# Optimization experiments

Measured on AMD Instinct MI355X. Metric: run time of the kernel, lower is better.

The kernel has to match this reference:

```python
import jax, jax.numpy as jnp
import numpy as np

H = W = 32
CROP = int(H * 0.8)  # 25, matches int(H*crop_ratio) in torch
MEAN = jnp.array([0.5071, 0.4867, 0.4408], jnp.float32).reshape(1, 3, 1, 1)
STD = jnp.array([0.2675, 0.2565, 0.2761], jnp.float32).reshape(1, 3, 1, 1)


def _bilinear(img, iy, ix):
    # img [C,H,W]; iy/ix [H,W] float pixel coords (reflected+clamped already)
    y0 = jnp.floor(iy); x0 = jnp.floor(ix)
    wy = iy - y0; wx = ix - x0
    y0i = jnp.clip(y0.astype(jnp.int32), 0, H - 1); y1i = jnp.clip(y0i + 1, 0, H - 1)
    x0i = jnp.clip(x0.astype(jnp.int32), 0, W - 1); x1i = jnp.clip(x0i + 1, 0, W - 1)
    v00 = img[:, y0i, x0i]; v01 = img[:, y0i, x1i]
    v10 = img[:, y1i, x0i]; v11 = img[:, y1i, x1i]
    return v00 * (1 - wy) * (1 - wx) + v01 * (1 - wy) * wx + v10 * wy * (1 - wx) + v11 * wy * wx


def _reflect(c, size):
    # PyTorch grid_sample reflection padding, align_corners=False (reflect about -0.5 / size-0.5)
    lo = -0.5
    span = float(size)
    t = jnp.abs(c - lo)
    extra = jnp.mod(t, span)
    flips = jnp.floor(t / span)
    out = jnp.where(jnp.mod(flips, 2.0) == 0.0, lo + extra, lo + span - extra)
    return jnp.clip(out, 0.0, size - 1.0)


def _crop_resize_one(img, top, left):
    # bilinear resize of img[:, top:top+CROP, left:left+CROP] -> HxW, align_corners=False
    d = (jnp.arange(W, dtype=jnp.float32) + 0.5) * (CROP / W) - 0.5
    d = jnp.maximum(d, 0.0)
    i0 = jnp.floor(d).astype(jnp.int32)
    lam = d - i0
    i1 = jnp.minimum(i0 + 1, CROP - 1)
    r0 = top + i0; r1 = top + i1; c0 = left + i0; c1 = left + i1
    v00 = img[:, r0[:, None], c0[None, :]]
    v01 = img[:, r0[:, None], c1[None, :]]
    v10 = img[:, r1[:, None], c0[None, :]]
    v11 = img[:, r1[:, None], c1[None, :]]
    ly = lam[:, None]; lx = lam[None, :]
    return v00 * (1 - ly) * (1 - lx) + v01 * (1 - ly) * lx + v10 * ly * (1 - lx) + v11 * ly * lx


def _grid_sample_one(img, theta):
    # affine_grid + grid_sample (bilinear, reflection, align_corners=False)
    xs = (2.0 * (jnp.arange(W, dtype=jnp.float32) + 0.5) / W) - 1.0
    ys = (2.0 * (jnp.arange(H, dtype=jnp.float32) + 0.5) / H) - 1.0
    yn, xn = jnp.meshgrid(ys, xs, indexing='ij')
    gx = theta[0, 0] * xn + theta[0, 1] * yn + theta[0, 2]
    gy = theta[1, 0] * xn + theta[1, 1] * yn + theta[1, 2]
    ix = _reflect(((gx + 1.0) * W - 1.0) * 0.5, W)
    iy = _reflect(((gy + 1.0) * H - 1.0) * 0.5, H)
    return _bilinear(img, iy, ix)


def _augment(x, shared_affine, apply_crop):
    B = x.shape[0]
    ks = jax.random.split(jax.random.key(42), 10)
    x = x * STD + MEAN  # de-normalize
    if apply_crop:
        max_off = H - CROP
        top = jax.random.randint(ks[0], (B,), 0, max_off + 1)
        left = jax.random.randint(ks[1], (B,), 0, max_off + 1)
        x = jax.vmap(_crop_resize_one)(x, top, left)
    flip_mask = jax.random.uniform(ks[2], (B,)) < 0.5
    x = jnp.where(flip_mask[:, None, None, None], x[..., ::-1], x)
    # shared affine is provided -> always applied (torch shared_affine branch)
    x = jax.vmap(_grid_sample_one)(x, shared_affine)
    brightness = 1.0 + (jax.random.uniform(ks[3], (B, 1, 1, 1)) - 0.5) * 0.8
    x = x * brightness
    gray = x.mean(axis=1, keepdims=True)
    contrast = 1.0 + (jax.random.uniform(ks[4], (B, 1, 1, 1)) - 0.5) * 0.8
    x = gray + (x - gray) * contrast
    gray = x.mean(axis=1, keepdims=True)
    saturation = 1.0 + (jax.random.uniform(ks[5], (B, 1, 1, 1)) - 0.5) * 0.8
    x = gray + (x - gray) * saturation
    hue_mask = jax.random.uniform(ks[6], (B,)) < 0.5
    x = jnp.where(hue_mask[:, None, None, None], x[:, ::-1], x)  # BGR swap
    gray_mask = jax.random.uniform(ks[7], (B,)) < 0.2
    x = jnp.where(gray_mask[:, None, None, None], x.mean(axis=1, keepdims=True), x)
    blur_mask = jax.random.uniform(ks[8], (B,)) < 0.5
    xp = jnp.pad(x, ((0, 0), (0, 0), (1, 1), (1, 1)), mode='edge')  # replicate pad
    bl = sum(xp[:, :, i:i + H, j:j + W] for i in range(3) for j in range(3)) / 9.0  # 3x3 box blur
    x = jnp.where(blur_mask[:, None, None, None], bl, x)
    solar_mask = jax.random.uniform(ks[9], (B,)) < 0.1
    x = jnp.where(solar_mask[:, None, None, None] & (x > 0.5), 1.0 - x, x)
    x = jnp.clip(x, 0.0, 1.0)
    x = (x - MEAN) / STD  # re-normalize
    return x, flip_mask


def setup_inputs() -> dict:
    key = jax.random.key(0)
    k1, k2 = jax.random.split(key)
    B = 8192
    x = jax.random.normal(k1, (B, 3, H, W), jnp.float32)
    eye = jnp.broadcast_to(jnp.array([[1.0, 0.0, 0.0], [0.0, 1.0, 0.0]], jnp.float32), (B, 2, 3))
    shared_affine = eye + 0.1 * jax.random.normal(k2, (B, 2, 3), jnp.float32)
    return {"x": x, "shared_affine": shared_affine, "apply_crop": 1}


def reference(x, shared_affine, apply_crop):
    out, flip_mask = _augment(x, shared_affine, int(apply_crop))
    # torch returns (x, {'flip': flip_mask, 'affine': affine_theta})
    return out, flip_mask, shared_affine
```

## Files before the change

### kernel.cpp

```cpp
#include <hip/hip_runtime.h>

#define HW 32
#define NPIX 1024
#define IMG 3072

typedef float vf4 __attribute__((ext_vector_type(4)));

__device__ __forceinline__ unsigned rotl32(unsigned x, int d) {
    return (x << d) | (x >> (32 - d));
}

struct UPair { unsigned a, b; };

__device__ __forceinline__ UPair threefry2x32(unsigned k0, unsigned k1,
                                              unsigned x0, unsigned x1) {
    unsigned k2 = k0 ^ k1 ^ 0x1BD11BDAu;
    x0 += k0; x1 += k1;
#define RND(r) { x0 += x1; x1 = rotl32(x1, (r)); x1 ^= x0; }
    RND(13) RND(15) RND(26) RND(6)
    x0 += k1; x1 += k2 + 1u;
    RND(17) RND(29) RND(16) RND(24)
    x0 += k2; x1 += k0 + 2u;
    RND(13) RND(15) RND(26) RND(6)
    x0 += k0; x1 += k1 + 3u;
    RND(17) RND(29) RND(16) RND(24)
    x0 += k1; x1 += k2 + 4u;
    RND(13) RND(15) RND(26) RND(6)
    x0 += k2; x1 += k0 + 5u;
#undef RND
    return {x0, x1};
}

__device__ __forceinline__ float bits_to_u01(unsigned bits) {
    return __uint_as_float((bits >> 9) | 0x3f800000u) - 1.0f;
}

__device__ __forceinline__ float reflect32(float c) {
    float t = fabsf(c + 0.5f);
    float flips = floorf(t * 0.03125f);
    float extra = fmaf(flips, -32.0f, t);
    float o = (((int)flips) & 1) ? (31.5f - extra) : (extra - 0.5f);
    return fminf(fmaxf(o, 0.0f), 31.0f);
}

__device__ __forceinline__ float rfl_f(float v) {
    return __uint_as_float(__builtin_amdgcn_readfirstlane(__float_as_uint(v)));
}
__device__ __forceinline__ int rfl_i(int v) {
    return __builtin_amdgcn_readfirstlane(v);
}

__global__ __launch_bounds__(64) void aug_kernel(
    const float* __restrict__ xin, const float* __restrict__ aff,
    const int* __restrict__ apply_crop, float* __restrict__ out, int B) {
    __shared__ vf4 buf[NPIX];
    __shared__ float s_theta[6];
    __shared__ int s_top, s_left, s_flip, s_hue, s_gray, s_blur, s_solar;
    __shared__ float s_bright, s_contr, s_sat;

    const int b = blockIdx.x;
    const int t = threadIdx.x;
    const bool do_crop = (apply_crop[0] != 0);

    const float* src = xin + (size_t)b * IMG;
    vf4 L0[4], L1[4], L2[4];
#pragma unroll
    for (int m = 0; m < 4; ++m) {
        int p = 256 * m + 4 * t;
        L0[m] = *(const vf4*)(src + p);
        L1[m] = *(const vf4*)(src + NPIX + p);
        L2[m] = *(const vf4*)(src + 2 * NPIX + p);
    }

    const size_t OUT_IMG = (size_t)B * IMG;
    if (t < 6) {
        float v = aff[b * 6 + t];
        s_theta[t] = v;
        out[OUT_IMG + (size_t)B + (size_t)b * 6 + t] = v;
    }

    if (t < 10) {
        int k = t;
        UPair K = threefry2x32(0u, 42u, 0u, (unsigned)k);
        if (k < 2) {
            UPair k2 = threefry2x32(K.a, K.b, 0u, 1u);
            UPair r = threefry2x32(k2.a, k2.b, 0u, (unsigned)b);
            int val = (int)((r.a ^ r.b) & 7u);
            if (k == 0) s_top = val; else s_left = val;
        } else {
            UPair r = threefry2x32(K.a, K.b, 0u, (unsigned)b);
            float u = bits_to_u01(r.a ^ r.b);
            if      (k == 2) s_flip  = (u < 0.5f);
            else if (k == 3) s_bright = 1.0f + (u - 0.5f) * 0.8f;
            else if (k == 4) s_contr  = 1.0f + (u - 0.5f) * 0.8f;
            else if (k == 5) s_sat    = 1.0f + (u - 0.5f) * 0.8f;
            else if (k == 6) s_hue   = (u < 0.5f);
            else if (k == 7) s_gray  = (u < 0.2f);
            else if (k == 8) s_blur  = (u < 0.5f);
            else             s_solar = (u < 0.1f);
        }
    }

#pragma unroll
    for (int m = 0; m < 4; ++m) {
        int p = 256 * m + 4 * t;
#pragma unroll
        for (int j = 0; j < 4; ++j) {
            vf4 v;
            v.x = fmaf(L0[m][j], 0.2675f, 0.5071f);
            v.y = fmaf(L1[m][j], 0.2565f, 0.4867f);
            v.z = fmaf(L2[m][j], 0.2761f, 0.4408f);
            v.w = 0.0f;
            buf[p + j] = v;
        }
    }

    if (t == 0) out[OUT_IMG + b] = s_flip ? 1.0f : 0.0f;
    const int top  = rfl_i(s_top),  left = rfl_i(s_left);
    const int flip = rfl_i(s_flip), hue  = rfl_i(s_hue);
    const int gray = rfl_i(s_gray), blur = rfl_i(s_blur), solar = rfl_i(s_solar);
    const float br   = rfl_f(s_bright);
    const float ctsa = rfl_f(s_contr) * rfl_f(s_sat);
    const float th0 = rfl_f(s_theta[0]), th1 = rfl_f(s_theta[1]), th2 = rfl_f(s_theta[2]);
    const float th3 = rfl_f(s_theta[3]), th4 = rfl_f(s_theta[4]), th5 = rfl_f(s_theta[5]);

    float cx[16], cy[16], cz[16];

    if (do_crop) {
#pragma unroll
        for (int m = 0; m < 4; ++m) {
#pragma unroll
            for (int j = 0; j < 4; ++j) {
                const int i = 4 * m + j;
                int p = 256 * m + 4 * t + j;
                int yi = p >> 5, xj = p & 31;
                float dy = fmaxf(fmaf((float)yi, 0.78125f, -0.109375f), 0.0f);
                int i0 = (int)dy; float ly = dy - (float)i0; int i1 = min(i0 + 1, 24);
                float dx = fmaxf(fmaf((float)xj, 0.78125f, -0.109375f), 0.0f);
                int q0 = (int)dx; float lx = dx - (float)q0; int q1 = min(q0 + 1, 24);
                int r0 = (top + i0) << 5, r1 = (top + i1) << 5;
                int c0 = left + q0, c1 = left + q1;
                float omy = 1.0f - ly, omx = 1.0f - lx;
                float w00 = omy * omx, w01 = omy * lx;
                float w10 = ly * omx, w11 = ly * lx;
                vf4 t00 = buf[r0 + c0], t01 = buf[r0 + c1];
                vf4 t10 = buf[r1 + c0], t11 = buf[r1 + c1];
                cx[i] = fmaf(t00.x, w00, fmaf(t01.x, w01, fmaf(t10.x, w10, t11.x * w11)));
                cy[i] = fmaf(t00.y, w00, fmaf(t01.y, w01, fmaf(t10.y, w10, t11.y * w11)));
                cz[i] = fmaf(t00.z, w00, fmaf(t01.z, w01, fmaf(t10.z, w10, t11.z * w11)));
            }
        }
#pragma unroll
        for (int m = 0; m < 4; ++m) {
#pragma unroll
            for (int j = 0; j < 4; ++j) {
                const int i = 4 * m + j;
                int p = 256 * m + 4 * t + j;
                vf4 v; v.x = cx[i]; v.y = cy[i]; v.z = cz[i]; v.w = 0.0f;
                buf[p] = v;
            }
        }
    }

#pragma unroll
    for (int m = 0; m < 4; ++m) {
#pragma unroll
        for (int j = 0; j < 4; ++j) {
            const int i = 4 * m + j;
            int p = 256 * m + 4 * t + j;
            int yi = p >> 5, xj = p & 31;
            float xn = (float)xj * 0.0625f - 0.96875f;
            float yn = (float)yi * 0.0625f - 0.96875f;
            float gx = fmaf(th0, xn, fmaf(th1, yn, th2));
            float gy = fmaf(th3, xn, fmaf(th4, yn, th5));
            float ix = reflect32(fmaf(gx, 16.0f, 15.5f));
            float iy = reflect32(fmaf(gy, 16.0f, 15.5f));
            float fy = floorf(iy), fx = floorf(ix);
            float wy = iy - fy, wx = ix - fx;
            int y0 = (int)fy; int y1 = min(y0 + 1, 31);
            int x0 = (int)fx; int x1 = min(x0 + 1, 31);
            if (flip) { x0 = 31 - x0; x1 = 31 - x1; }
            int r0 = y0 << 5, r1 = y1 << 5;
            float omy = 1.0f - wy, omx = 1.0f - wx;
            float w00 = omy * omx, w01 = omy * wx;
            float w10 = wy * omx, w11 = wy * wx;
            vf4 t00 = buf[r0 + x0], t01 = buf[r0 + x1];
            vf4 t10 = buf[r1 + x0], t11 = buf[r1 + x1];
            float ch0 = fmaf(t00.x, w00, fmaf(t01.x, w01, fmaf(t10.x, w10, t11.x * w11)));
            float ch1 = fmaf(t00.y, w00, fmaf(t01.y, w01, fmaf(t10.y, w10, t11.y * w11)));
            float ch2 = fmaf(t00.z, w00, fmaf(t01.z, w01, fmaf(t10.z, w10, t11.z * w11)));
            ch0 *= br; ch1 *= br; ch2 *= br;
            float g = (ch0 + ch1 + ch2) * (1.0f / 3.0f);
            ch0 = fmaf(ch0 - g, ctsa, g);
            ch1 = fmaf(ch1 - g, ctsa, g);
            ch2 = fmaf(ch2 - g, ctsa, g);
            if (hue) { float tmp = ch0; ch0 = ch2; ch2 = tmp; }
            if (gray) { ch0 = ch1 = ch2 = g; }
            cx[i] = ch0; cy[i] = ch1; cz[i] = ch2;
        }
    }

    if (blur) {
        const int le = ((t & 7) == 0), re = ((t & 7) == 7);
        const int tl = (t - 1) & 63, tr = (t + 1) & 63;
#pragma unroll
        for (int m = 0; m < 4; ++m) {
            const int q = 4 * m;
            {
                float v0 = cx[q], v1 = cx[q+1], v2 = cx[q+2], v3 = cx[q+3];
                float lf = __shfl(v3, tl), rt = __shfl(v0, tr);
                if (le) lf = v0;  if (re) rt = v3;
                float s01 = v0 + v1, s23 = v2 + v3;
                cx[q] = lf + s01; cx[q+1] = s01 + v2; cx[q+2] = v1 + s23; cx[q+3] = s23 + rt;
            }
            {
                float v0 = cy[q], v1 = cy[q+1], v2 = cy[q+2], v3 = cy[q+3];
                float lf = __shfl(v3, tl), rt = __shfl(v0, tr);
                if (le) lf = v0;  if (re) rt = v3;
                float s01 = v0 + v1, s23 = v2 + v3;
                cy[q] = lf + s01; cy[q+1] = s01 + v2; cy[q+2] = v1 + s23; cy[q+3] = s23 + rt;
            }
            {
                float v0 = cz[q], v1 = cz[q+1], v2 = cz[q+2], v3 = cz[q+3];
                float lf = __shfl(v3, tl), rt = __shfl(v0, tr);
                if (le) lf = v0;  if (re) rt = v3;
                float s01 = v0 + v1, s23 = v2 + v3;
                cz[q] = lf + s01; cz[q+1] = s01 + v2; cz[q+2] = v1 + s23; cz[q+3] = s23 + rt;
            }
        }
#pragma unroll
        for (int m = 0; m < 4; ++m) {
#pragma unroll
            for (int j = 0; j < 4; ++j) {
                const int i = 4 * m + j;
                int p = 256 * m + 4 * t + j;
                vf4 v; v.x = cx[i]; v.y = cy[i]; v.z = cz[i]; v.w = 0.0f;
                buf[p] = v;
            }
        }
#pragma unroll
        for (int m = 0; m < 4; ++m) {
#pragma unroll
            for (int j = 0; j < 4; ++j) {
                const int i = 4 * m + j;
                int p = 256 * m + 4 * t + j;
                int yi = p >> 5, xj = p & 31;
                vf4 up = buf[(max(yi - 1, 0) << 5) + xj];
                vf4 dn = buf[(min(yi + 1, 31) << 5) + xj];
                cx[i] = (up.x + cx[i] + dn.x) * (1.0f / 9.0f);
                cy[i] = (up.y + cy[i] + dn.y) * (1.0f / 9.0f);
                cz[i] = (up.z + cz[i] + dn.z) * (1.0f / 9.0f);
            }
        }
    }

    {
        const float INV0 = 1.0f / 0.2675f, INV1 = 1.0f / 0.2565f, INV2 = 1.0f / 0.2761f;
        float* o = out + (size_t)b * IMG;
#pragma unroll
        for (int m = 0; m < 4; ++m) {
            int p = 256 * m + 4 * t;
            vf4 o0, o1, o2;
#pragma unroll
            for (int j = 0; j < 4; ++j) {
                const int i = 4 * m + j;
                float r0v = cx[i], r1v = cy[i], r2v = cz[i];
                if (solar) {
                    if (r0v > 0.5f) r0v = 1.0f - r0v;
                    if (r1v > 0.5f) r1v = 1.0f - r1v;
                    if (r2v > 0.5f) r2v = 1.0f - r2v;
                }
                r0v = fminf(fmaxf(r0v, 0.0f), 1.0f);
                r1v = fminf(fmaxf(r1v, 0.0f), 1.0f);
                r2v = fminf(fmaxf(r2v, 0.0f), 1.0f);
                o0[j] = (r0v - 0.5071f) * INV0;
                o1[j] = (r1v - 0.4867f) * INV1;
                o2[j] = (r2v - 0.4408f) * INV2;
            }
            *(vf4*)(o + p) = o0;
            *(vf4*)(o + NPIX + p) = o1;
            *(vf4*)(o + 2 * NPIX + p) = o2;
        }
    }
}

extern "C" void kernel_launch(void* const* d_in, const int* in_sizes, int n_in,
                              void* d_out, int out_size, void* d_ws, size_t ws_size,
                              hipStream_t stream) {
    const float* x = (const float*)d_in[0];
    const float* aff = (const float*)d_in[1];
    const int* ac = (const int*)d_in[2];
    float* out = (float*)d_out;
    int B = in_sizes[0] / IMG;
    aug_kernel<<<dim3(B), dim3(64), 0, stream>>>(x, aff, ac, out, B);
}
```

Before: 195.1 us.

## Use 256 threads per image with one pixel column per thread and block syncs

Each block now runs 256 threads instead of one 64-thread wave. Each thread owns four pixels in one column (rows yr+8i) instead of sixteen, and loads and stores are scalar and coalesced instead of float4. __syncthreads barriers are added between the shared-memory stages because the block spans several waves. The horizontal blur now uses per-pixel shuffles across 32-lane rows. The aim is more parallelism and lower register pressure per thread, in exchange for barrier cost and narrower memory accesses.

```diff
diff --git a/kernel.cpp b/kernel.cpp
--- a/kernel.cpp
+++ b/kernel.cpp
@@ -50,7 +50,7 @@
     return __builtin_amdgcn_readfirstlane(v);
 }
 
-__global__ __launch_bounds__(64) void aug_kernel(
+__global__ __launch_bounds__(256) void aug_kernel(
     const float* __restrict__ xin, const float* __restrict__ aff,
     const int* __restrict__ apply_crop, float* __restrict__ out, int B) {
     __shared__ vf4 buf[NPIX];
@@ -60,16 +60,18 @@
 
     const int b = blockIdx.x;
     const int t = threadIdx.x;
+    const int x = t & 31;
+    const int yr = t >> 5;
     const bool do_crop = (apply_crop[0] != 0);
 
     const float* src = xin + (size_t)b * IMG;
-    vf4 L0[4], L1[4], L2[4];
-#pragma unroll
-    for (int m = 0; m < 4; ++m) {
-        int p = 256 * m + 4 * t;
-        L0[m] = *(const vf4*)(src + p);
-        L1[m] = *(const vf4*)(src + NPIX + p);
-        L2[m] = *(const vf4*)(src + 2 * NPIX + p);
+    float g0[4], g1[4], g2[4];
+#pragma unroll
+    for (int i = 0; i < 4; ++i) {
+        int p = t + 256 * i;
+        g0[i] = src[p];
+        g1[i] = src[NPIX + p];
+        g2[i] = src[2 * NPIX + p];
     }
 
     const size_t OUT_IMG = (size_t)B * IMG;
@@ -102,18 +104,15 @@
     }
 
 #pragma unroll
-    for (int m = 0; m < 4; ++m) {
-        int p = 256 * m + 4 * t;
-#pragma unroll
-        for (int j = 0; j < 4; ++j) {
-            vf4 v;
-            v.x = fmaf(L0[m][j], 0.2675f, 0.5071f);
-            v.y = fmaf(L1[m][j], 0.2565f, 0.4867f);
-            v.z = fmaf(L2[m][j], 0.2761f, 0.4408f);
-            v.w = 0.0f;
-            buf[p + j] = v;
-        }
-    }
+    for (int i = 0; i < 4; ++i) {
+        vf4 v;
+        v.x = fmaf(g0[i], 0.2675f, 0.5071f);
+        v.y = fmaf(g1[i], 0.2565f, 0.4867f);
+        v.z = fmaf(g2[i], 0.2761f, 0.4408f);
+        v.w = 0.0f;
+        buf[t + 256 * i] = v;
+    }
+    __syncthreads();
 
     if (t == 0) out[OUT_IMG + b] = s_flip ? 1.0f : 0.0f;
     const int top  = rfl_i(s_top),  left = rfl_i(s_left);
@@ -124,52 +123,42 @@
     const float th0 = rfl_f(s_theta[0]), th1 = rfl_f(s_theta[1]), th2 = rfl_f(s_theta[2]);
     const float th3 = rfl_f(s_theta[3]), th4 = rfl_f(s_theta[4]), th5 = rfl_f(s_theta[5]);
 
-    float cx[16], cy[16], cz[16];
+    float cx[4], cy[4], cz[4];
 
     if (do_crop) {
-#pragma unroll
-        for (int m = 0; m < 4; ++m) {
-#pragma unroll
-            for (int j = 0; j < 4; ++j) {
-                const int i = 4 * m + j;
-                int p = 256 * m + 4 * t + j;
-                int yi = p >> 5, xj = p & 31;
-                float dy = fmaxf(fmaf((float)yi, 0.78125f, -0.109375f), 0.0f);
-                int i0 = (int)dy; float ly = dy - (float)i0; int i1 = min(i0 + 1, 24);
-                float dx = fmaxf(fmaf((float)xj, 0.78125f, -0.109375f), 0.0f);
-                int q0 = (int)dx; float lx = dx - (float)q0; int q1 = min(q0 + 1, 24);
-                int r0 = (top + i0) << 5, r1 = (top + i1) << 5;
-                int c0 = left + q0, c1 = left + q1;
-                float omy = 1.0f - ly, omx = 1.0f - lx;
-                float w00 = omy * omx, w01 = omy * lx;
-                float w10 = ly * omx, w11 = ly * lx;
-                vf4 t00 = buf[r0 + c0], t01 = buf[r0 + c1];
-                vf4 t10 = buf[r1 + c0], t11 = buf[r1 + c1];
-                cx[i] = fmaf(t00.x, w00, fmaf(t01.x, w01, fmaf(t10.x, w10, t11.x * w11)));
-                cy[i] = fmaf(t00.y, w00, fmaf(t01.y, w01, fmaf(t10.y, w10, t11.y * w11)));
-                cz[i] = fmaf(t00.z, w00, fmaf(t01.z, w01, fmaf(t10.z, w10, t11.z * w11)));
-            }
-        }
-#pragma unroll
-        for (int m = 0; m < 4; ++m) {
-#pragma unroll
-            for (int j = 0; j < 4; ++j) {
-                const int i = 4 * m + j;
-                int p = 256 * m + 4 * t + j;
-                vf4 v; v.x = cx[i]; v.y = cy[i]; v.z = cz[i]; v.w = 0.0f;
-                buf[p] = v;
-            }
-        }
-    }
-
-#pragma unroll
-    for (int m = 0; m < 4; ++m) {
-#pragma unroll
-        for (int j = 0; j < 4; ++j) {
-            const int i = 4 * m + j;
-            int p = 256 * m + 4 * t + j;
-            int yi = p >> 5, xj = p & 31;
-            float xn = (float)xj * 0.0625f - 0.96875f;
+        float dxv = fmaxf(fmaf((float)x, 0.78125f, -0.109375f), 0.0f);
+        int q0 = (int)dxv; float lx = dxv - (float)q0; int q1 = min(q0 + 1, 24);
+        int c0 = left + q0, c1 = left + q1;
+        float omx = 1.0f - lx;
+#pragma unroll
+        for (int i = 0; i < 4; ++i) {
+            int yi = yr + 8 * i;
+            float dy = fmaxf(fmaf((float)yi, 0.78125f, -0.109375f), 0.0f);
+            int i0 = (int)dy; float ly = dy - (float)i0; int i1 = min(i0 + 1, 24);
+            int r0 = (top + i0) << 5, r1 = (top + i1) << 5;
+            float omy = 1.0f - ly;
+            float w00 = omy * omx, w01 = omy * lx;
+            float w10 = ly * omx, w11 = ly * lx;
+            vf4 t00 = buf[r0 + c0], t01 = buf[r0 + c1];
+            vf4 t10 = buf[r1 + c0], t11 = buf[r1 + c1];
+            cx[i] = fmaf(t00.x, w00, fmaf(t01.x, w01, fmaf(t10.x, w10, t11.x * w11)));
+            cy[i] = fmaf(t00.y, w00, fmaf(t01.y, w01, fmaf(t10.y, w10, t11.y * w11)));
+            cz[i] = fmaf(t00.z, w00, fmaf(t01.z, w01, fmaf(t10.z, w10, t11.z * w11)));
+        }
+        __syncthreads();
+#pragma unroll
+        for (int i = 0; i < 4; ++i) {
+            vf4 v; v.x = cx[i]; v.y = cy[i]; v.z = cz[i]; v.w = 0.0f;
+            buf[t + 256 * i] = v;
+        }
+        __syncthreads();
+    }
+
+    {
+        float xn = (float)x * 0.0625f - 0.96875f;
+#pragma unroll
+        for (int i = 0; i < 4; ++i) {
+            int yi = yr + 8 * i;
             float yn = (float)yi * 0.0625f - 0.96875f;
             float gx = fmaf(th0, xn, fmaf(th1, yn, th2));
             float gy = fmaf(th3, xn, fmaf(th4, yn, th5));
@@ -201,56 +190,36 @@
     }
 
     if (blur) {
-        const int le = ((t & 7) == 0), re = ((t & 7) == 7);
-        const int tl = (t - 1) & 63, tr = (t + 1) & 63;
-#pragma unroll
-        for (int m = 0; m < 4; ++m) {
-            const int q = 4 * m;
-            {
-                float v0 = cx[q], v1 = cx[q+1], v2 = cx[q+2], v3 = cx[q+3];
-                float lf = __shfl(v3, tl), rt = __shfl(v0, tr);
-                if (le) lf = v0;  if (re) rt = v3;
-                float s01 = v0 + v1, s23 = v2 + v3;
-                cx[q] = lf + s01; cx[q+1] = s01 + v2; cx[q+2] = v1 + s23; cx[q+3] = s23 + rt;
-            }
-            {
-                float v0 = cy[q], v1 = cy[q+1], v2 = cy[q+2], v3 = cy[q+3];
-                float lf = __shfl(v3, tl), rt = __shfl(v0, tr);
-                if (le) lf = v0;  if (re) rt = v3;
-                float s01 = v0 + v1, s23 = v2 + v3;
-                cy[q] = lf + s01; cy[q+1] = s01 + v2; cy[q+2] = v1 + s23; cy[q+3] = s23 + rt;
-            }
-            {
-                float v0 = cz[q], v1 = cz[q+1], v2 = cz[q+2], v3 = cz[q+3];
-                float lf = __shfl(v3, tl), rt = __shfl(v0, tr);
-                if (le) lf = v0;  if (re) rt = v3;
-                float s01 = v0 + v1, s23 = v2 + v3;
-                cz[q] = lf + s01; cz[q+1] = s01 + v2; cz[q+2] = v1 + s23; cz[q+3] = s23 + rt;
-            }
-        }
-#pragma unroll
-        for (int m = 0; m < 4; ++m) {
-#pragma unroll
-            for (int j = 0; j < 4; ++j) {
-                const int i = 4 * m + j;
-                int p = 256 * m + 4 * t + j;
-                vf4 v; v.x = cx[i]; v.y = cy[i]; v.z = cz[i]; v.w = 0.0f;
-                buf[p] = v;
-            }
-        }
-#pragma unroll
-        for (int m = 0; m < 4; ++m) {
-#pragma unroll
-            for (int j = 0; j < 4; ++j) {
-                const int i = 4 * m + j;
-                int p = 256 * m + 4 * t + j;
-                int yi = p >> 5, xj = p & 31;
-                vf4 up = buf[(max(yi - 1, 0) << 5) + xj];
-                vf4 dn = buf[(min(yi + 1, 31) << 5) + xj];
-                cx[i] = (up.x + cx[i] + dn.x) * (1.0f / 9.0f);
-                cy[i] = (up.y + cy[i] + dn.y) * (1.0f / 9.0f);
-                cz[i] = (up.z + cz[i] + dn.z) * (1.0f / 9.0f);
-            }
+        __syncthreads();
+        const int tl = t - 1, tr = t + 1;
+        float hx[4], hy[4], hz[4];
+#pragma unroll
+        for (int i = 0; i < 4; ++i) {
+            float v, lf, rt;
+            v = cx[i]; lf = __shfl(v, tl); rt = __shfl(v, tr);
+            if (x == 0) lf = v;  if (x == 31) rt = v;
+            hx[i] = lf + v + rt;
+            v = cy[i]; lf = __shfl(v, tl); rt = __shfl(v, tr);
+            if (x == 0) lf = v;  if (x == 31) rt = v;
+            hy[i] = lf + v + rt;
+            v = cz[i]; lf = __shfl(v, tl); rt = __shfl(v, tr);
+            if (x == 0) lf = v;  if (x == 31) rt = v;
+            hz[i] = lf + v + rt;
+        }
+#pragma unroll
+        for (int i = 0; i < 4; ++i) {
+            vf4 v; v.x = hx[i]; v.y = hy[i]; v.z = hz[i]; v.w = 0.0f;
+            buf[t + 256 * i] = v;
+        }
+        __syncthreads();
+#pragma unroll
+        for (int i = 0; i < 4; ++i) {
+            int yi = yr + 8 * i;
+            vf4 up = buf[(max(yi - 1, 0) << 5) + x];
+            vf4 dn = buf[(min(yi + 1, 31) << 5) + x];
+            cx[i] = (up.x + hx[i] + dn.x) * (1.0f / 9.0f);
+            cy[i] = (up.y + hy[i] + dn.y) * (1.0f / 9.0f);
+            cz[i] = (up.z + hz[i] + dn.z) * (1.0f / 9.0f);
         }
     }
 
@@ -258,28 +227,20 @@
         const float INV0 = 1.0f / 0.2675f, INV1 = 1.0f / 0.2565f, INV2 = 1.0f / 0.2761f;
         float* o = out + (size_t)b * IMG;
 #pragma unroll
-        for (int m = 0; m < 4; ++m) {
-            int p = 256 * m + 4 * t;
-            vf4 o0, o1, o2;
-#pragma unroll
-            for (int j = 0; j < 4; ++j) {
-                const int i = 4 * m + j;
-                float r0v = cx[i], r1v = cy[i], r2v = cz[i];
-                if (solar) {
-                    if (r0v > 0.5f) r0v = 1.0f - r0v;
-                    if (r1v > 0.5f) r1v = 1.0f - r1v;
-                    if (r2v > 0.5f) r2v = 1.0f - r2v;
-                }
-                r0v = fminf(fmaxf(r0v, 0.0f), 1.0f);
-                r1v = fminf(fmaxf(r1v, 0.0f), 1.0f);
-                r2v = fminf(fmaxf(r2v, 0.0f), 1.0f);
-                o0[j] = (r0v - 0.5071f) * INV0;
-                o1[j] = (r1v - 0.4867f) * INV1;
-                o2[j] = (r2v - 0.4408f) * INV2;
+        for (int i = 0; i < 4; ++i) {
+            int p = t + 256 * i;
+            float r0v = cx[i], r1v = cy[i], r2v = cz[i];
+            if (solar) {
+                if (r0v > 0.5f) r0v = 1.0f - r0v;
+                if (r1v > 0.5f) r1v = 1.0f - r1v;
+                if (r2v > 0.5f) r2v = 1.0f - r2v;
             }
-            *(vf4*)(o + p) = o0;
-            *(vf4*)(o + NPIX + p) = o1;
-            *(vf4*)(o + 2 * NPIX + p) = o2;
+            r0v = fminf(fmaxf(r0v, 0.0f), 1.0f);
+            r1v = fminf(fmaxf(r1v, 0.0f), 1.0f);
+            r2v = fminf(fmaxf(r2v, 0.0f), 1.0f);
+            o[p]             = (r0v - 0.5071f) * INV0;
+            o[NPIX + p]      = (r1v - 0.4867f) * INV1;
+            o[2 * NPIX + p]  = (r2v - 0.4408f) * INV2;
         }
     }
 }
@@ -292,5 +253,5 @@
     const int* ac = (const int*)d_in[2];
     float* out = (float*)d_out;
     int B = in_sizes[0] / IMG;
-    aug_kernel<<<dim3(B), dim3(64), 0, stream>>>(x, aff, ac, out, B);
-}
+    aug_kernel<<<dim3(B), dim3(256), 0, stream>>>(x, aff, ac, out, B);
+}
```

Measured after the change: 182.3 us. 1.07x faster.
